# Kernel optimization log

Measured on AMD Instinct MI355X. Metric: run time of the kernel, lower is better.

## Reference

```python
import jax, jax.numpy as jnp
import numpy as np
from math import pi as PI

N_NODES = 50000
N_EDGES = 1000000
HIDDEN = 128
N_GAUSS = 50
N_FILT = 128
N_COLORS = 4
CUTOFF = 10.0
LOG2 = float(np.log(2.0))


def setup_inputs() -> dict:
    key = jax.random.key(0)
    ks = jax.random.split(key, 16)
    glorot = jax.nn.initializers.glorot_uniform()
    inp = {
        "x": jax.random.normal(ks[0], (N_NODES, HIDDEN), jnp.float32),
        "edge_index": jax.random.randint(ks[1], (2, N_EDGES), 0, N_NODES),
        "edge_weight": jax.random.uniform(ks[2], (N_EDGES,), jnp.float32) * CUTOFF,
        "edge_attr": jax.random.normal(ks[3], (N_EDGES, N_GAUSS), jnp.float32),
        "colors": jax.random.randint(ks[4], (N_EDGES,), 0, N_COLORS),
        # ColoredMLP params, stacked over colors
        "mlp1_w": glorot(ks[5], (N_COLORS, N_FILT, N_GAUSS), jnp.float32),
        "mlp1_b": jnp.zeros((N_COLORS, N_FILT), jnp.float32),
        "mlp2_w": glorot(ks[6], (N_COLORS, N_FILT, N_FILT), jnp.float32),
        "mlp2_b": jnp.zeros((N_COLORS, N_FILT), jnp.float32),
        # CFConv linears
        "lin1_w": glorot(ks[7], (N_FILT, HIDDEN), jnp.float32),
        "lin2_w": glorot(ks[8], (HIDDEN, N_FILT), jnp.float32),
        "lin2_b": jnp.zeros((HIDDEN,), jnp.float32),
        # final Linear
        "lin_w": glorot(ks[9], (HIDDEN, HIDDEN), jnp.float32),
        "lin_b": jnp.zeros((HIDDEN,), jnp.float32),
    }
    return inp


def shifted_softplus(v):
    return jax.nn.softplus(v) - LOG2


def colored_mlp(edge_attr, colors, mlp1_w, mlp1_b, mlp2_w, mlp2_b):
    # per-color small MLP; loop over the small fixed color set, select by mask
    out = jnp.zeros((edge_attr.shape[0], N_FILT), edge_attr.dtype)
    for c in range(N_COLORS):
        h = shifted_softplus(edge_attr @ mlp1_w[c].T + mlp1_b[c])
        h = h @ mlp2_w[c].T + mlp2_b[c]
        out = jnp.where((colors == c)[:, None], h, out)
    return out


def reference(x, edge_index, edge_weight, edge_attr, colors,
              mlp1_w, mlp1_b, mlp2_w, mlp2_b,
              lin1_w, lin2_w, lin2_b, lin_w, lin_b):
    # cosine cutoff
    C = 0.5 * (jnp.cos(edge_weight * PI / CUTOFF) + 1.0)  # [E]
    W = colored_mlp(edge_attr, colors, mlp1_w, mlp1_b, mlp2_w, mlp2_b) * C[:, None]  # [E,F]
    h = x @ lin1_w.T  # [N,F]
    src, dst = edge_index[0], edge_index[1]
    msg = h[src] * W  # gather + modulate, [E,F]
    agg = jax.ops.segment_sum(msg, dst, num_segments=N_NODES)  # scatter-add, [N,F]
    out = agg @ lin2_w.T + lin2_b  # [N,H]
    out = shifted_softplus(out)
    out = out @ lin_w.T + lin_b
    return out
```

## Files before the change

### kernel.cpp

```cpp
#include <hip/hip_runtime.h>
#include <math.h>

#define N_NODES_ 50000
#define N_EDGES_ 1000000
#define HID 128
#define NG 50
#define NF 128
#define NCOL 4
#define CSEG 258048
#define NKEY (NCOL * N_NODES_)
#define CHUNK 625
#define NCHUNK_PER_C 80
#define NCHUNK (NCOL * NCHUNK_PER_C)

typedef short s16x8 __attribute__((ext_vector_type(8)));
typedef float f32x4 __attribute__((ext_vector_type(4)));

__device__ __forceinline__ float sspf(float v) {
    float r = __logf(1.f + __expf(v)) - 0.69314718055994531f;
    return (v > 15.f) ? (v - 0.69314718055994531f) : r;
}

__device__ __forceinline__ unsigned int f2b(float f) {
    unsigned int u = __float_as_uint(f);
    return (u + 0x7fffu + ((u >> 16) & 1u)) >> 16;
}

__global__ __launch_bounds__(256) void hist_kernel(const int* __restrict__ colors,
                                                   const int* __restrict__ edge_index,
                                                   int* __restrict__ hist) {
    int e = blockIdx.x * 256 + threadIdx.x;
    if (e < N_EDGES_) {
        int key = colors[e] * N_NODES_ + edge_index[N_EDGES_ + e];
        atomicAdd(&hist[key], 1);
    }
}

__global__ __launch_bounds__(256) void scan1_kernel(int* __restrict__ hist,
                                                    int* __restrict__ csum) {
    __shared__ int s[CHUNK];
    int b = blockIdx.x;
    int c = b / NCHUNK_PER_C, ch = b % NCHUNK_PER_C;
    int gofs = c * N_NODES_ + ch * CHUNK;
    for (int i = threadIdx.x; i < CHUNK; i += 256) s[i] = hist[gofs + i];
    __syncthreads();
    if (threadIdx.x == 0) {
        int run = 0;
        for (int i = 0; i < CHUNK; ++i) { int t = s[i]; s[i] = run; run += t; }
        csum[b] = run;
    }
    __syncthreads();
    for (int i = threadIdx.x; i < CHUNK; i += 256) hist[gofs + i] = s[i];
}

__global__ __launch_bounds__(64) void scan2_kernel(const int* __restrict__ csum,
                                                   int* __restrict__ cbase,
                                                   int* __restrict__ g_cnt) {
    int c = threadIdx.x;
    if (c < NCOL) {
        int run = 0;
        for (int j = 0; j < NCHUNK_PER_C; ++j) {
            cbase[c * NCHUNK_PER_C + j] = run;
            run += csum[c * NCHUNK_PER_C + j];
        }
        g_cnt[c] = run;
    }
}

__global__ __launch_bounds__(256) void scan3_kernel(int* __restrict__ hist,
                                                    const int* __restrict__ cbase) {
    int b = blockIdx.x;
    int c = b / NCHUNK_PER_C, ch = b % NCHUNK_PER_C;
    int gofs = c * N_NODES_ + ch * CHUNK;
    int add = cbase[b];
    for (int i = threadIdx.x; i < CHUNK; i += 256) hist[gofs + i] += add;
}

__global__ __launch_bounds__(256) void scatter_kernel(const int* __restrict__ colors,
                                                      const int* __restrict__ edge_index,
                                                      int* __restrict__ base,
                                                      int* __restrict__ eid_s) {
    int e = blockIdx.x * 256 + threadIdx.x;
    if (e < N_EDGES_) {
        int c = colors[e];
        int key = c * N_NODES_ + edge_index[N_EDGES_ + e];
        int r = atomicAdd(&base[key], 1);
        eid_s[c * CSEG + r] = e;
    }
}

__global__ __launch_bounds__(256) void wconv_kernel(const float* __restrict__ m1w,
                                                    const float* __restrict__ m2w,
                                                    unsigned short* __restrict__ m1b16,
                                                    unsigned short* __restrict__ m2b16) {
    int idx = blockIdx.x * 256 + threadIdx.x;
    if (idx < NCOL * NF * 64) {
        int c = idx / (NF * 64);
        int rem = idx % (NF * 64);
        int n = rem / 64, k = rem % 64;
        float v = (k < NG) ? m1w[(c * NF + n) * NG + k] : 0.f;
        m1b16[idx] = (unsigned short)f2b(v);
    } else if (idx < NCOL * NF * 64 + NCOL * NF * NF) {
        int j = idx - NCOL * NF * 64;
        int cn = j / NF;
        int k = j % NF;
        int ks = k >> 5, qk = (k >> 3) & 3, jj = k & 7;
        int tau = ((2 * ks + (jj >> 2)) << 4) | (qk << 2) | (jj & 3);
        m2b16[j] = (unsigned short)f2b(m2w[cn * NF + tau]);
    }
}

__global__ __launch_bounds__(256, 8) void passA_kernel(
    const int* __restrict__ edge_index, const float* __restrict__ edge_weight,
    const float* __restrict__ edge_attr,
    const unsigned short* __restrict__ m1b16, const unsigned short* __restrict__ m2b16,
    const float* __restrict__ m1bias, const float* __restrict__ m2bias,
    const float* __restrict__ h, const int* __restrict__ eid_s,
    const int* __restrict__ g_cnt, float* __restrict__ agg) {

    int c = blockIdx.x >> 12;
    int tile = blockIdx.x & 4095;
    int cnt = g_cnt[c];
    if (tile * 64 >= cnt) return;
    int pos0 = c * CSEG + tile * 64;

    int tid = threadIdx.x;
    int wv = tid >> 6;
    int l15 = tid & 15;
    int q = (tid >> 4) & 3;
    int e = (wv << 4) | l15;

    int eid = eid_s[pos0 + e];
    int sidx = 0, d = -1;
    float cw = 0.f;
    if (eid >= 0) {
        sidx = edge_index[eid];
        d = edge_index[N_EDGES_ + eid];
        float ww = edge_weight[eid];
        cw = 0.5f * (__cosf(ww * 0.31415926535897932f) + 1.f);
    }

    union { s16x8 v; unsigned int u[4]; } bf0, bf1;
    {
        const float* ear = edge_attr + (size_t)((eid >= 0) ? eid : 0) * NG;
        float2 a0 = *(const float2*)(ear + q * 8 + 0);
        float2 a1 = *(const float2*)(ear + q * 8 + 2);
        float2 a2 = *(const float2*)(ear + q * 8 + 4);
        float2 a3 = *(const float2*)(ear + q * 8 + 6);
        bf0.u[0] = f2b(a0.x) | (f2b(a0.y) << 16);
        bf0.u[1] = f2b(a1.x) | (f2b(a1.y) << 16);
        bf0.u[2] = f2b(a2.x) | (f2b(a2.y) << 16);
        bf0.u[3] = f2b(a3.x) | (f2b(a3.y) << 16);
        float2 c0 = make_float2(0.f, 0.f), c1 = c0, c2 = c0, c3 = c0;
        int k1 = 32 + q * 8;
        if (q < 2) {
            c0 = *(const float2*)(ear + k1 + 0);
            c1 = *(const float2*)(ear + k1 + 2);
            c2 = *(const float2*)(ear + k1 + 4);
            c3 = *(const float2*)(ear + k1 + 6);
        } else if (q == 2) {
            c0 = *(const float2*)(ear + 48);
        }
        bf1.u[0] = f2b(c0.x) | (f2b(c0.y) << 16);
        bf1.u[1] = f2b(c1.x) | (f2b(c1.y) << 16);
        bf1.u[2] = f2b(c2.x) | (f2b(c2.y) << 16);
        bf1.u[3] = f2b(c3.x) | (f2b(c3.y) << 16);
    }

    uint2 p[8];
    {
        const unsigned short* m1p = m1b16 + (size_t)c * NF * 64;
        const float* b1p = m1bias + c * NF;
#pragma unroll
        for (int m = 0; m < 8; ++m) {
            f32x4 a = (f32x4)(0.f);
            s16x8 af0 = *(const s16x8*)(m1p + (m * 16 + l15) * 64 + q * 8);
            a = __builtin_amdgcn_mfma_f32_16x16x32_bf16(af0, bf0.v, a, 0, 0, 0);
            s16x8 af1 = *(const s16x8*)(m1p + (m * 16 + l15) * 64 + q * 8 + 32);
            a = __builtin_amdgcn_mfma_f32_16x16x32_bf16(af1, bf1.v, a, 0, 0, 0);
            int n0 = m * 16 + q * 4;
            f32x4 bv = *(const f32x4*)(b1p + n0);
            float t0 = sspf(a[0] + bv[0]);
            float t1 = sspf(a[1] + bv[1]);
            float t2 = sspf(a[2] + bv[2]);
            float t3 = sspf(a[3] + bv[3]);
            p[m].x = f2b(t0) | (f2b(t1) << 16);
            p[m].y = f2b(t2) | (f2b(t3) << 16);
        }
    }

    int dprev = __shfl_up(d, 1, 16);
    int dn1 = __shfl_down(d, 1, 16);
    int dn2 = __shfl_down(d, 2, 16);
    int dn4 = __shfl_down(d, 4, 16);
    int dn8 = __shfl_down(d, 8, 16);
    bool s1 = (dn1 == d) && (l15 + 1 < 16);
    bool s2 = (dn2 == d) && (l15 + 2 < 16);
    bool s4 = (dn4 == d) && (l15 + 4 < 16);
    bool s8 = (dn8 == d) && (l15 + 8 < 16);
    bool head = (d >= 0) && (l15 == 0 || d != dprev);

    const unsigned short* m2p = m2b16 + (size_t)c * NF * NF;
    const float* b2p = m2bias + c * NF;
    const float* hrow = h + (size_t)sidx * HID;
    float* ap = agg + (size_t)((d >= 0) ? d : 0) * HID + (q << 2);

#pragma unroll
    for (int m = 0; m < 8; ++m) {
        f32x4 a2 = (f32x4)(0.f);
#pragma unroll
        for (int ks = 0; ks < 4; ++ks) {
            union { s16x8 v; unsigned int u[4]; } bfr;
            bfr.u[0] = p[2 * ks].x;
            bfr.u[1] = p[2 * ks].y;
            bfr.u[2] = p[2 * ks + 1].x;
            bfr.u[3] = p[2 * ks + 1].y;
            s16x8 af = *(const s16x8*)(m2p + (m * 16 + l15) * NF + q * 8 + 32 * ks);
            a2 = __builtin_amdgcn_mfma_f32_16x16x32_bf16(af, bfr.v, a2, 0, 0, 0);
        }
        int n0 = m * 16 + q * 4;
        f32x4 hv = *(const f32x4*)(hrow + n0);
        f32x4 bv = *(const f32x4*)(b2p + n0);
        a2[0] = (a2[0] + bv[0]) * cw * hv[0];
        a2[1] = (a2[1] + bv[1]) * cw * hv[1];
        a2[2] = (a2[2] + bv[2]) * cw * hv[2];
        a2[3] = (a2[3] + bv[3]) * cw * hv[3];

#define SSTEP(sflag, dd)                                                     \
        {                                                                    \
            float v0 = __shfl_down(a2[0], dd, 16);                           \
            float v1 = __shfl_down(a2[1], dd, 16);                           \
            float v2 = __shfl_down(a2[2], dd, 16);                           \
            float v3 = __shfl_down(a2[3], dd, 16);                           \
            if (sflag) { a2[0] += v0; a2[1] += v1; a2[2] += v2; a2[3] += v3; } \
        }
        SSTEP(s1, 1)
        SSTEP(s2, 2)
        SSTEP(s4, 4)
        SSTEP(s8, 8)
#undef SSTEP

        if (head) {
            atomicAdd(ap + m * 16 + 0, a2[0]);
            atomicAdd(ap + m * 16 + 1, a2[1]);
            atomicAdd(ap + m * 16 + 2, a2[2]);
            atomicAdd(ap + m * 16 + 3, a2[3]);
        }
    }
}

__device__ __forceinline__ void fma_2x8(float (&acc)[2][8], float2 a, float4 b0, float4 b1) {
    acc[0][0] += a.x * b0.x; acc[0][1] += a.x * b0.y;
    acc[0][2] += a.x * b0.z; acc[0][3] += a.x * b0.w;
    acc[0][4] += a.x * b1.x; acc[0][5] += a.x * b1.y;
    acc[0][6] += a.x * b1.z; acc[0][7] += a.x * b1.w;
    acc[1][0] += a.y * b0.x; acc[1][1] += a.y * b0.y;
    acc[1][2] += a.y * b0.z; acc[1][3] += a.y * b0.w;
    acc[1][4] += a.y * b1.x; acc[1][5] += a.y * b1.y;
    acc[1][6] += a.y * b1.z; acc[1][7] += a.y * b1.w;
}

__device__ __forceinline__ void load_wT32(const float4* __restrict__ w4, int kc,
                                          float (*wT)[132], int tid) {
#pragma unroll
    for (int i = 0; i < 4; ++i) {
        int lin = tid + 256 * i;
        int col = lin >> 3;
        int m = lin & 7;
        float4 v = w4[col * 32 + (kc >> 2) + m];
        wT[4 * m + 0][col] = v.x;
        wT[4 * m + 1][col] = v.y;
        wT[4 * m + 2][col] = v.z;
        wT[4 * m + 3][col] = v.w;
    }
}

__global__ __launch_bounds__(256) void lin1_kernel(const float* __restrict__ x,
                                                   const float* __restrict__ w,
                                                   float* __restrict__ h) {
    __shared__ float xT[HID][36];
    __shared__ float wT[32][132];
    int tid = threadIdx.x;
    int tx = tid & 15, ty = tid >> 4;
    int r0 = blockIdx.x * 32;
    const float4* x4 = (const float4*)x;
#pragma unroll
    for (int i = 0; i < 4; ++i) {
        int lin = tid + 256 * i;
        int r = lin >> 5, m = lin & 31;
        int rr = r0 + r; if (rr > N_NODES_ - 1) rr = N_NODES_ - 1;
        float4 v = x4[rr * 32 + m];
        xT[4 * m + 0][r] = v.x; xT[4 * m + 1][r] = v.y;
        xT[4 * m + 2][r] = v.z; xT[4 * m + 3][r] = v.w;
    }
    float acc[2][8] = {};
    for (int kc = 0; kc < HID; kc += 32) {
        __syncthreads();
        load_wT32((const float4*)w, kc, wT, tid);
        __syncthreads();
#pragma unroll 8
        for (int k2 = 0; k2 < 32; ++k2) {
            float2 a = *(const float2*)&xT[kc + k2][2 * ty];
            float4 b0 = *(const float4*)&wT[k2][8 * tx];
            float4 b1 = *(const float4*)&wT[k2][8 * tx + 4];
            fma_2x8(acc, a, b0, b1);
        }
    }
    float4* h4 = (float4*)h;
#pragma unroll
    for (int i = 0; i < 2; ++i) {
        int row = r0 + 2 * ty + i;
        if (row < N_NODES_) {
            h4[row * 32 + 2 * tx]     = make_float4(acc[i][0], acc[i][1], acc[i][2], acc[i][3]);
            h4[row * 32 + 2 * tx + 1] = make_float4(acc[i][4], acc[i][5], acc[i][6], acc[i][7]);
        }
    }
}

__global__ __launch_bounds__(256) void out_kernel(
    const float* __restrict__ agg,
    const float* __restrict__ w2, const float* __restrict__ b2,
    const float* __restrict__ w3, const float* __restrict__ b3,
    float* __restrict__ out) {
    __shared__ float sT[HID][36];
    __shared__ float wT[32][132];
    int tid = threadIdx.x;
    int tx = tid & 15, ty = tid >> 4;
    int r0 = blockIdx.x * 32;
    const float4* a4 = (const float4*)agg;
#pragma unroll
    for (int i = 0; i < 4; ++i) {
        int lin = tid + 256 * i;
        int r = lin >> 5, m = lin & 31;
        int rr = r0 + r; if (rr > N_NODES_ - 1) rr = N_NODES_ - 1;
        float4 v = a4[rr * 32 + m];
        sT[4 * m + 0][r] = v.x; sT[4 * m + 1][r] = v.y;
        sT[4 * m + 2][r] = v.z; sT[4 * m + 3][r] = v.w;
    }
    float acc[2][8] = {};
    for (int kc = 0; kc < HID; kc += 32) {
        __syncthreads();
        load_wT32((const float4*)w2, kc, wT, tid);
        __syncthreads();
#pragma unroll 8
        for (int k2 = 0; k2 < 32; ++k2) {
            float2 a = *(const float2*)&sT[kc + k2][2 * ty];
            float4 c0 = *(const float4*)&wT[k2][8 * tx];
            float4 c1 = *(const float4*)&wT[k2][8 * tx + 4];
            fma_2x8(acc, a, c0, c1);
        }
    }
    __syncthreads();
#pragma unroll
    for (int j = 0; j < 8; ++j) {
        int col = 8 * tx + j;
        float bbv = b2[col];
        sT[col][2 * ty]     = sspf(acc[0][j] + bbv);
        sT[col][2 * ty + 1] = sspf(acc[1][j] + bbv);
    }
    float acc2[2][8] = {};
    for (int kc = 0; kc < HID; kc += 32) {
        __syncthreads();
        load_wT32((const float4*)w3, kc, wT, tid);
        __syncthreads();
#pragma unroll 8
        for (int k2 = 0; k2 < 32; ++k2) {
            float2 a = *(const float2*)&sT[kc + k2][2 * ty];
            float4 c0 = *(const float4*)&wT[k2][8 * tx];
            float4 c1 = *(const float4*)&wT[k2][8 * tx + 4];
            fma_2x8(acc2, a, c0, c1);
        }
    }
    float4* out4 = (float4*)out;
#pragma unroll
    for (int i = 0; i < 2; ++i) {
        int row = r0 + 2 * ty + i;
        if (row < N_NODES_) {
            out4[row * 32 + 2 * tx] = make_float4(
                acc2[i][0] + b3[8 * tx + 0], acc2[i][1] + b3[8 * tx + 1],
                acc2[i][2] + b3[8 * tx + 2], acc2[i][3] + b3[8 * tx + 3]);
            out4[row * 32 + 2 * tx + 1] = make_float4(
                acc2[i][4] + b3[8 * tx + 4], acc2[i][5] + b3[8 * tx + 5],
                acc2[i][6] + b3[8 * tx + 6], acc2[i][7] + b3[8 * tx + 7]);
        }
    }
}

extern "C" void kernel_launch(void* const* d_in, const int* in_sizes, int n_in,
                              void* d_out, int out_size, void* d_ws, size_t ws_size,
                              hipStream_t stream) {
    const float* x           = (const float*)d_in[0];
    const int*   edge_index  = (const int*)d_in[1];
    const float* edge_weight = (const float*)d_in[2];
    const float* edge_attr   = (const float*)d_in[3];
    const int*   colors      = (const int*)d_in[4];
    const float* m1w         = (const float*)d_in[5];
    const float* m1b         = (const float*)d_in[6];
    const float* m2w         = (const float*)d_in[7];
    const float* m2b         = (const float*)d_in[8];
    const float* lin1w       = (const float*)d_in[9];
    const float* lin2w       = (const float*)d_in[10];
    const float* lin2b       = (const float*)d_in[11];
    const float* linw        = (const float*)d_in[12];
    const float* linb        = (const float*)d_in[13];
    float* out = (float*)d_out;

    char* ws = (char*)d_ws;
    float* h      = (float*)(ws);
    float* agg    = (float*)(ws + 25600000);
    int*   eid_s  = (int*)(ws + 51200000);
    int*   base   = (int*)(ws + 55328768);
    int*   csum   = (int*)(ws + 56128768);
    int*   cbase  = (int*)(ws + 56130048);
    int*   g_cnt  = (int*)(ws + 56131328);
    unsigned short* m1b16 = (unsigned short*)(ws + 56131392);
    unsigned short* m2b16 = (unsigned short*)(ws + 56196928);

    hipMemsetAsync(agg, 0, (size_t)N_NODES_ * HID * sizeof(float), stream);
    hipMemsetAsync(base, 0, NKEY * sizeof(int), stream);
    hipMemsetAsync(eid_s, 0xFF, (size_t)NCOL * CSEG * sizeof(int), stream);

    hist_kernel<<<(N_EDGES_ + 255) / 256, 256, 0, stream>>>(colors, edge_index, base);
    scan1_kernel<<<NCHUNK, 256, 0, stream>>>(base, csum);
    scan2_kernel<<<1, 64, 0, stream>>>(csum, cbase, g_cnt);
    scan3_kernel<<<NCHUNK, 256, 0, stream>>>(base, cbase);
    scatter_kernel<<<(N_EDGES_ + 255) / 256, 256, 0, stream>>>(colors, edge_index, base, eid_s);
    wconv_kernel<<<(NCOL * NF * 64 + NCOL * NF * NF + 255) / 256, 256, 0, stream>>>(m1w, m2w, m1b16, m2b16);
    lin1_kernel<<<(N_NODES_ + 31) / 32, 256, 0, stream>>>(x, lin1w, h);
    passA_kernel<<<NCOL * 4096, 256, 0, stream>>>(edge_index, edge_weight, edge_attr,
                                                  m1b16, m2b16, m1b, m2b, h, eid_s, g_cnt, agg);
    out_kernel<<<(N_NODES_ + 31) / 32, 256, 0, stream>>>(agg, lin2w, lin2b, linw, linb, out);
}
```

Before: 1.048 ms.

## Stage per-color MLP2 weights in swizzled LDS and presort dst/cutoff per edge

The scatter kernel now also writes the destination index and cosine cutoff weight into the color/destination-sorted slot order, so passA reads them contiguously instead of gathering edge_index and edge_weight by edge id. passA copies the color's bf16 second-layer weight matrix into 32KB of XOR-swizzled shared memory and feeds the MFMA A operands from LDS rather than from global memory. This trades extra global writes, an extra memset, a per-block 32KB weight load and lower occupancy for cheaper, bank-conflict-free weight fetches and fewer random gathers.

```diff
diff --git a/kernel.cpp b/kernel.cpp
--- a/kernel.cpp
+++ b/kernel.cpp
@@ -78,14 +78,21 @@
 
 __global__ __launch_bounds__(256) void scatter_kernel(const int* __restrict__ colors,
                                                       const int* __restrict__ edge_index,
+                                                      const float* __restrict__ edge_weight,
                                                       int* __restrict__ base,
-                                                      int* __restrict__ eid_s) {
+                                                      int* __restrict__ eid_s,
+                                                      int* __restrict__ dst_s,
+                                                      float* __restrict__ cw_s) {
     int e = blockIdx.x * 256 + threadIdx.x;
     if (e < N_EDGES_) {
         int c = colors[e];
-        int key = c * N_NODES_ + edge_index[N_EDGES_ + e];
+        int d = edge_index[N_EDGES_ + e];
+        int key = c * N_NODES_ + d;
         int r = atomicAdd(&base[key], 1);
-        eid_s[c * CSEG + r] = e;
+        int slot = c * CSEG + r;
+        eid_s[slot] = e;
+        dst_s[slot] = d;
+        cw_s[slot] = 0.5f * (__cosf(edge_weight[e] * 0.31415926535897932f) + 1.f);
     }
 }
 
@@ -110,13 +117,16 @@
     }
 }
 
-__global__ __launch_bounds__(256, 8) void passA_kernel(
-    const int* __restrict__ edge_index, const float* __restrict__ edge_weight,
+__global__ __launch_bounds__(256, 4) void passA_kernel(
+    const int* __restrict__ edge_index,
     const float* __restrict__ edge_attr,
     const unsigned short* __restrict__ m1b16, const unsigned short* __restrict__ m2b16,
     const float* __restrict__ m1bias, const float* __restrict__ m2bias,
     const float* __restrict__ h, const int* __restrict__ eid_s,
+    const int* __restrict__ dst_s, const float* __restrict__ cw_s,
     const int* __restrict__ g_cnt, float* __restrict__ agg) {
+
+    __shared__ __align__(16) char sm2[32768];
 
     int c = blockIdx.x >> 12;
     int tile = blockIdx.x & 4095;
@@ -130,15 +140,23 @@
     int q = (tid >> 4) & 3;
     int e = (wv << 4) | l15;
 
+    {
+        const uint4* g4 = (const uint4*)(m2b16 + (size_t)c * NF * NF);
+#pragma unroll
+        for (int i = 0; i < 8; ++i) {
+            int c0 = tid + 256 * i;
+            int row = c0 >> 4;
+            int k0 = c0 & 15;
+            int dstb = row * 256 + ((k0 * 16) ^ ((row & 7) << 4));
+            *(uint4*)(sm2 + dstb) = g4[c0];
+        }
+    }
+
     int eid = eid_s[pos0 + e];
-    int sidx = 0, d = -1;
-    float cw = 0.f;
-    if (eid >= 0) {
-        sidx = edge_index[eid];
-        d = edge_index[N_EDGES_ + eid];
-        float ww = edge_weight[eid];
-        cw = 0.5f * (__cosf(ww * 0.31415926535897932f) + 1.f);
-    }
+    int d = dst_s[pos0 + e];
+    float cw = cw_s[pos0 + e];
+    int sidx = 0;
+    if (eid >= 0) sidx = edge_index[eid];
 
     union { s16x8 v; unsigned int u[4]; } bf0, bf1;
     {
@@ -200,14 +218,18 @@
     bool s8 = (dn8 == d) && (l15 + 8 < 16);
     bool head = (d >= 0) && (l15 == 0 || d != dprev);
 
-    const unsigned short* m2p = m2b16 + (size_t)c * NF * NF;
+    __syncthreads();
+
     const float* b2p = m2bias + c * NF;
     const float* hrow = h + (size_t)sidx * HID;
     float* ap = agg + (size_t)((d >= 0) ? d : 0) * HID + (q << 2);
+    int rowb0 = l15 * 256;
+    int sw = (l15 & 7) << 4;
 
 #pragma unroll
     for (int m = 0; m < 8; ++m) {
         f32x4 a2 = (f32x4)(0.f);
+        const char* rp = sm2 + rowb0 + m * 4096;
 #pragma unroll
         for (int ks = 0; ks < 4; ++ks) {
             union { s16x8 v; unsigned int u[4]; } bfr;
@@ -215,7 +237,7 @@
             bfr.u[1] = p[2 * ks].y;
             bfr.u[2] = p[2 * ks + 1].x;
             bfr.u[3] = p[2 * ks + 1].y;
-            s16x8 af = *(const s16x8*)(m2p + (m * 16 + l15) * NF + q * 8 + 32 * ks);
+            s16x8 af = *(const s16x8*)(rp + ((q * 16 + ks * 64) ^ sw));
             a2 = __builtin_amdgcn_mfma_f32_16x16x32_bf16(af, bfr.v, a2, 0, 0, 0);
         }
         int n0 = m * 16 + q * 4;
@@ -409,25 +431,30 @@
     float* h      = (float*)(ws);
     float* agg    = (float*)(ws + 25600000);
     int*   eid_s  = (int*)(ws + 51200000);
-    int*   base   = (int*)(ws + 55328768);
-    int*   csum   = (int*)(ws + 56128768);
-    int*   cbase  = (int*)(ws + 56130048);
-    int*   g_cnt  = (int*)(ws + 56131328);
-    unsigned short* m1b16 = (unsigned short*)(ws + 56131392);
-    unsigned short* m2b16 = (unsigned short*)(ws + 56196928);
+    int*   dst_s  = (int*)(ws + 55328768);
+    float* cw_s   = (float*)(ws + 59457536);
+    int*   base   = (int*)(ws + 63586304);
+    int*   csum   = (int*)(ws + 64386304);
+    int*   cbase  = (int*)(ws + 64387584);
+    int*   g_cnt  = (int*)(ws + 64388864);
+    unsigned short* m1b16 = (unsigned short*)(ws + 64388928);
+    unsigned short* m2b16 = (unsigned short*)(ws + 64454464);
 
     hipMemsetAsync(agg, 0, (size_t)N_NODES_ * HID * sizeof(float), stream);
     hipMemsetAsync(base, 0, NKEY * sizeof(int), stream);
     hipMemsetAsync(eid_s, 0xFF, (size_t)NCOL * CSEG * sizeof(int), stream);
+    hipMemsetAsync(dst_s, 0xFF, (size_t)NCOL * CSEG * sizeof(int), stream);
 
     hist_kernel<<<(N_EDGES_ + 255) / 256, 256, 0, stream>>>(colors, edge_index, base);
     scan1_kernel<<<NCHUNK, 256, 0, stream>>>(base, csum);
     scan2_kernel<<<1, 64, 0, stream>>>(csum, cbase, g_cnt);
     scan3_kernel<<<NCHUNK, 256, 0, stream>>>(base, cbase);
-    scatter_kernel<<<(N_EDGES_ + 255) / 256, 256, 0, stream>>>(colors, edge_index, base, eid_s);
+    scatter_kernel<<<(N_EDGES_ + 255) / 256, 256, 0, stream>>>(colors, edge_index, edge_weight,
+                                                               base, eid_s, dst_s, cw_s);
     wconv_kernel<<<(NCOL * NF * 64 + NCOL * NF * NF + 255) / 256, 256, 0, stream>>>(m1w, m2w, m1b16, m2b16);
     lin1_kernel<<<(N_NODES_ + 31) / 32, 256, 0, stream>>>(x, lin1w, h);
-    passA_kernel<<<NCOL * 4096, 256, 0, stream>>>(edge_index, edge_weight, edge_attr,
-                                                  m1b16, m2b16, m1b, m2b, h, eid_s, g_cnt, agg);
+    passA_kernel<<<NCOL * 4096, 256, 0, stream>>>(edge_index, edge_attr,
+                                                  m1b16, m2b16, m1b, m2b, h, eid_s,
+                                                  dst_s, cw_s, g_cnt, agg);
     out_kernel<<<(N_NODES_ + 31) / 32, 256, 0, stream>>>(agg, lin2w, lin2b, linw, linb, out);
 }
```

Result: faster. 980.3 us (-6.5%).
